# Performance work log

Hardware: AMD Instinct MI355X
Metric: run time of the kernel (lower is better)

Reference implementation:

```python
import jax, jax.numpy as jnp
import numpy as np

B, S, H, NH, FF, L = 2, 2048, 768, 12, 3072, 2
DH = H // NH
EPS = 1e-12
NEG = -10000.0


def setup_inputs() -> dict:
    key = jax.random.key(0)
    ks = jax.random.split(key, 10)
    w = lambda k, shp: jax.random.normal(k, shp, dtype=jnp.float32) * 0.02
    return {
        'hidden_states': jax.random.normal(ks[0], (B, S, H), dtype=jnp.float32),
        'attention_mask': jnp.ones((B, S), jnp.float32),
        'bias_matrix': jax.random.normal(ks[1], (S, S), dtype=jnp.float32) * 0.1,
        'bias_coef': jnp.ones((), jnp.float32),
        'Wq': w(ks[2], (L, H, H)), 'bq': jnp.zeros((L, H), jnp.float32),
        'Wk': w(ks[3], (L, H, H)), 'bk': jnp.zeros((L, H), jnp.float32),
        'Wv': w(ks[4], (L, H, H)), 'bv': jnp.zeros((L, H), jnp.float32),
        'Wo': w(ks[5], (L, H, H)), 'bo': jnp.zeros((L, H), jnp.float32),
        'ln1_g': jnp.ones((L, H), jnp.float32), 'ln1_b': jnp.zeros((L, H), jnp.float32),
        'Wi': w(ks[6], (L, H, FF)), 'bi': jnp.zeros((L, FF), jnp.float32),
        'Wo2': w(ks[7], (L, FF, H)), 'bo2': jnp.zeros((L, H), jnp.float32),
        'ln2_g': jnp.ones((L, H), jnp.float32), 'ln2_b': jnp.zeros((L, H), jnp.float32),
    }


def _layer_norm(x, g, b):
    mu = jnp.mean(x, axis=-1, keepdims=True)
    var = jnp.mean(jnp.square(x - mu), axis=-1, keepdims=True)
    return (x - mu) * jax.lax.rsqrt(var + EPS) * g + b


def reference(hidden_states, attention_mask, bias_matrix, bias_coef,
              Wq, bq, Wk, bk, Wv, bv, Wo, bo, ln1_g, ln1_b,
              Wi, bi, Wo2, bo2, ln2_g, ln2_b):
    # extended additive mask: [B,1,1,S]
    ext_mask = (1.0 - attention_mask)[:, None, None, :] * NEG
    bias = bias_matrix[None, None] * bias_coef  # [1,1,S,S]
    x = hidden_states
    scale = 1.0 / np.sqrt(DH)
    for i in range(L):
        q = (x @ Wq[i] + bq[i]).reshape(B, S, NH, DH).transpose(0, 2, 1, 3)
        k = (x @ Wk[i] + bk[i]).reshape(B, S, NH, DH).transpose(0, 2, 1, 3)
        v = (x @ Wv[i] + bv[i]).reshape(B, S, NH, DH).transpose(0, 2, 1, 3)
        scores = jnp.einsum('bhqd,bhkd->bhqk', q, k) * scale
        scores = scores + bias + ext_mask
        probs = jax.nn.softmax(scores, axis=-1)  # dropout = identity (eval)
        ctx = jnp.einsum('bhqk,bhkd->bhqd', probs, v)
        ctx = ctx.transpose(0, 2, 1, 3).reshape(B, S, H)
        attn_out = ctx @ Wo[i] + bo[i]
        x = _layer_norm(attn_out + x, ln1_g[i], ln1_b[i])
        inter = jax.nn.gelu(x @ Wi[i] + bi[i], approximate=False)
        ffn_out = inter @ Wo2[i] + bo2[i]
        x = _layer_norm(ffn_out + x, ln2_g[i], ln2_b[i])
    return x
```

## Files before the change

kernel.cpp:

```cpp
#include <hip/hip_runtime.h>
#include <hip/hip_bf16.h>
#include <math.h>

#define BB     2
#define SS     2048
#define HH     768
#define NHEAD  12
#define DHEAD  64
#define FFD    3072
#define NLAYER 2
#define MTOK   (BB*SS)
#define LOG2E  1.4426950408889634f
#define QSCALE 0.18033688011112042f

typedef __attribute__((ext_vector_type(8))) short bf16x8;
typedef __attribute__((ext_vector_type(4))) short bf16x4;
typedef __attribute__((ext_vector_type(4))) float f32x4;

__device__ __forceinline__ short f2bs(float f) {
    union { float f; unsigned u; } v; v.f = f;
    unsigned r = v.u + 0x7FFF + ((v.u >> 16) & 1);
    return (short)(r >> 16);
}
__device__ __forceinline__ float bs2f(short s) {
    union { unsigned u; float f; } v; v.u = ((unsigned)(unsigned short)s) << 16;
    return v.f;
}
__device__ __forceinline__ float fexp2(float x) {
    float r; asm("v_exp_f32 %0, %1" : "=v"(r) : "v"(x)); return r;
}
__device__ __forceinline__ void gl2lds16(const short* g, short* l) {
    __builtin_amdgcn_global_load_lds(
        (const __attribute__((address_space(1))) unsigned int*)g,
        (__attribute__((address_space(3))) unsigned int*)l, 16, 0, 0);
}

struct TJobs { const float* src[8]; short* dst[8]; };

__global__ __launch_bounds__(256)
void transpose_cvt_batch(TJobs jobs, int K, int N)
{
    const float* __restrict__ W  = jobs.src[blockIdx.z];
    short* __restrict__ Wt = jobs.dst[blockIdx.z];
    __shared__ short tile[32][33];
    const int k0 = blockIdx.x * 32, n0 = blockIdx.y * 32;
    const int tx = threadIdx.x & 31, ty = threadIdx.x >> 5;
#pragma unroll
    for (int i = 0; i < 4; i++)
        tile[ty + i*8][tx] = f2bs(W[(size_t)(k0 + ty + i*8) * N + n0 + tx]);
    __syncthreads();
#pragma unroll
    for (int i = 0; i < 4; i++)
        Wt[(size_t)(n0 + ty + i*8) * K + k0 + tx] = tile[tx][ty + i*8];
}

__global__ __launch_bounds__(256)
void cvt_bf16(const float* __restrict__ src, short* __restrict__ dst, int n)
{
    const int i = blockIdx.x * 256 + threadIdx.x;
    if (i < n) dst[i] = f2bs(src[i]);
}

__global__ __launch_bounds__(256)
void pack_bias(const float* __restrict__ bq, const float* __restrict__ bk,
               const float* __restrict__ bv, float* __restrict__ bqkv)
{
    const int t = blockIdx.x * 256 + threadIdx.x;
    if (t >= NLAYER * 2304) return;
    const int l = t / 2304, r = t % 2304;
    const float* src = (r < 768) ? bq : (r < 1536 ? bk : bv);
    bqkv[t] = src[l*768 + (r % 768)];
}

__global__ __launch_bounds__(256)
void bias_frag_prep(const float* __restrict__ biasM, const float* __restrict__ mask,
                    const float* __restrict__ coefp, short* __restrict__ bFrag)
{
    __shared__ float tile[64][129];
    const int tid = threadIdx.x;
    const int qb = blockIdx.x, q0 = qb*64, k0 = blockIdx.y*128;
#pragma unroll
    for (int p = 0; p < 8; p++) {
        const int row = p*8 + (tid >> 5);
        const int col = (tid & 31) * 4;
        float4 v = *(const float4*)&biasM[(size_t)(q0 + row)*SS + k0 + col];
        tile[row][col+0] = v.x; tile[row][col+1] = v.y;
        tile[row][col+2] = v.z; tile[row][col+3] = v.w;
    }
    __syncthreads();
    const float coef = coefp[0];
    const int lane = tid & 63, w = tid >> 6;
    const int l16 = lane & 15, g = lane >> 4;
    const int qrow = w*16 + l16;
#pragma unroll
    for (int b = 0; b < BB; b++) {
#pragma unroll
        for (int kt = 0; kt < 8; kt++) {
            bf16x4 o;
#pragma unroll
            for (int r = 0; r < 4; r++) {
                const int kk = kt*16 + g*4 + r;
                const float madd = (1.f - mask[b*SS + k0 + kk]) * (-10000.0f);
                o[r] = f2bs((tile[qrow][kk] * coef + madd) * LOG2E);
            }
            const size_t idx = ((((size_t)b*32 + qb)*4 + w)*128 + (k0>>4) + kt)*256 + lane*4;
            *(bf16x4*)&bFrag[idx] = o;
        }
    }
}

__global__ __launch_bounds__(256)
void gemm_mfma(const short* __restrict__ A, const short* __restrict__ Bt,
               const float* __restrict__ bias, short* __restrict__ C, int ldc,
               int M, int N, int K, int gelu, short* __restrict__ VtOut, int vsplit,
               float qscale, int qcols)
{
    __shared__ short sA[2][128*32];
    __shared__ short sB[2][128*32];
    const int tid  = threadIdx.x;
    const int w    = tid >> 6;
    const int lane = tid & 63;
    const int l16  = lane & 15, g = lane >> 4;
    const int wm   = w & 1, wn = w >> 1;
    const size_t m0 = (size_t)blockIdx.y * 128, n0 = (size_t)blockIdx.x * 128;

    const int srow = lane >> 2;
    const int kc   = lane & 3;

    f32x4 acc[4][4];
#pragma unroll
    for (int i = 0; i < 4; i++)
#pragma unroll
        for (int j = 0; j < 4; j++) acc[i][j] = (f32x4){0.f,0.f,0.f,0.f};

    const short* gA0 = A  + (m0 + w*32 +      srow) * (size_t)K + kc*8;
    const short* gA1 = A  + (m0 + w*32 + 16 + srow) * (size_t)K + kc*8;
    const short* gB0 = Bt + (n0 + w*32 +      srow) * (size_t)K + kc*8;
    const short* gB1 = Bt + (n0 + w*32 + 16 + srow) * (size_t)K + kc*8;
    const int oA0 = (w*32     )*32, oA1 = (w*32 + 16)*32;

    for (int k0 = 0; k0 < K; k0 += 64) {
        gl2lds16(gA0 + k0,      &sA[0][oA0]);
        gl2lds16(gA1 + k0,      &sA[0][oA1]);
        gl2lds16(gB0 + k0,      &sB[0][oA0]);
        gl2lds16(gB1 + k0,      &sB[0][oA1]);
        gl2lds16(gA0 + k0 + 32, &sA[1][oA0]);
        gl2lds16(gA1 + k0 + 32, &sA[1][oA1]);
        gl2lds16(gB0 + k0 + 32, &sB[1][oA0]);
        gl2lds16(gB1 + k0 + 32, &sB[1][oA1]);
        __syncthreads();

#pragma unroll
        for (int s = 0; s < 2; s++) {
            bf16x8 af[4], bfr[4];
#pragma unroll
            for (int mt = 0; mt < 4; mt++)
                af[mt] = *(const bf16x8*)&sA[s][(wm*64 + mt*16 + l16)*32 + g*8];
#pragma unroll
            for (int nt = 0; nt < 4; nt++)
                bfr[nt] = *(const bf16x8*)&sB[s][(wn*64 + nt*16 + l16)*32 + g*8];
#pragma unroll
            for (int mt = 0; mt < 4; mt++)
#pragma unroll
                for (int nt = 0; nt < 4; nt++)
                    acc[mt][nt] = __builtin_amdgcn_mfma_f32_16x16x32_bf16(
                                      af[mt], bfr[nt], acc[mt][nt], 0, 0, 0);
        }
        __syncthreads();
    }

#pragma unroll
    for (int mt = 0; mt < 4; mt++) {
        const size_t row0 = m0 + wm*64 + mt*16 + g*4;
#pragma unroll
        for (int nt = 0; nt < 4; nt++) {
            const size_t col = n0 + wn*64 + nt*16 + l16;
            if ((int)col >= vsplit) {
                short4 t;
                t.x = f2bs(acc[mt][nt][0] + bias[col]);
                t.y = f2bs(acc[mt][nt][1] + bias[col]);
                t.z = f2bs(acc[mt][nt][2] + bias[col]);
                t.w = f2bs(acc[mt][nt][3] + bias[col]);
                *(short4*)&VtOut[(size_t)(col - vsplit)*MTOK + row0] = t;
            } else {
#pragma unroll
                for (int r = 0; r < 4; r++) {
                    float v = acc[mt][nt][r] + bias[col];
                    if ((int)col < qcols) v *= qscale;
                    if (gelu) v = 0.5f * v * (1.f + erff(v * 0.70710678118f));
                    C[(row0 + r) * (size_t)ldc + col] = f2bs(v);
                }
            }
        }
    }
}

__global__ __launch_bounds__(256)
void gemm_n64_splitk(const short* __restrict__ A, const short* __restrict__ Bt,
                     float* __restrict__ P, int K)
{
    const int K2 = K >> 1;
    const int z  = blockIdx.z;
    __shared__ short sA[2][128*32];
    __shared__ short sB[2][64*32];
    const int tid  = threadIdx.x;
    const int w    = tid >> 6;
    const int lane = tid & 63;
    const int l16  = lane & 15, g = lane >> 4;
    const int wm   = w & 1, wn = w >> 1;
    const size_t m0 = (size_t)blockIdx.y * 128, n0 = (size_t)blockIdx.x * 64;

    const int srow = lane >> 2;
    const int kc   = lane & 3;

    f32x4 acc[4][2];
#pragma unroll
    for (int i = 0; i < 4; i++)
#pragma unroll
        for (int j = 0; j < 2; j++) acc[i][j] = (f32x4){0.f,0.f,0.f,0.f};

    const short* gA0 = A  + (m0 + w*32 +      srow) * (size_t)K + z*K2 + kc*8;
    const short* gA1 = A  + (m0 + w*32 + 16 + srow) * (size_t)K + z*K2 + kc*8;
    const short* gB0 = Bt + (n0 + w*16 +      srow) * (size_t)K + z*K2 + kc*8;
    const int oA0 = (w*32     )*32, oA1 = (w*32 + 16)*32, oB0 = (w*16)*32;

    for (int k0 = 0; k0 < K2; k0 += 64) {
        gl2lds16(gA0 + k0,      &sA[0][oA0]);
        gl2lds16(gA1 + k0,      &sA[0][oA1]);
        gl2lds16(gB0 + k0,      &sB[0][oB0]);
        gl2lds16(gA0 + k0 + 32, &sA[1][oA0]);
        gl2lds16(gA1 + k0 + 32, &sA[1][oA1]);
        gl2lds16(gB0 + k0 + 32, &sB[1][oB0]);
        __syncthreads();

#pragma unroll
        for (int s = 0; s < 2; s++) {
            bf16x8 af[4], bfr[2];
#pragma unroll
            for (int mt = 0; mt < 4; mt++)
                af[mt] = *(const bf16x8*)&sA[s][(wm*64 + mt*16 + l16)*32 + g*8];
#pragma unroll
            for (int nt = 0; nt < 2; nt++)
                bfr[nt] = *(const bf16x8*)&sB[s][(wn*32 + nt*16 + l16)*32 + g*8];
#pragma unroll
            for (int mt = 0; mt < 4; mt++)
#pragma unroll
                for (int nt = 0; nt < 2; nt++)
                    acc[mt][nt] = __builtin_amdgcn_mfma_f32_16x16x32_bf16(
                                      af[mt], bfr[nt], acc[mt][nt], 0, 0, 0);
        }
        __syncthreads();
    }

    float* Pz = P + (size_t)z * MTOK * HH;
#pragma unroll
    for (int mt = 0; mt < 4; mt++) {
        const size_t row0 = m0 + wm*64 + mt*16 + g*4;
#pragma unroll
        for (int nt = 0; nt < 2; nt++) {
            const size_t col = n0 + wn*32 + nt*16 + l16;
#pragma unroll
            for (int r = 0; r < 4; r++)
                Pz[(row0 + r) * (size_t)HH + col] = acc[mt][nt][r];
        }
    }
}

__global__ __launch_bounds__(256, 3)
void attn_fused(const short* __restrict__ QK, const short* __restrict__ Vt,
                const short* __restrict__ bFrag, short* __restrict__ CTX)
{
    __shared__ short sK[128*72];
    __shared__ short sV[64*136];

    const int qb  = blockIdx.x;
    const int q0  = qb * 64;
    const int h   = blockIdx.y;
    const int b   = blockIdx.z;
    const int tid = threadIdx.x;
    const int w   = tid >> 6;
    const int lane = tid & 63;
    const int l16 = lane & 15;
    const int g   = lane >> 4;

    const short* qrow = QK + ((size_t)(b*SS) + q0 + w*16 + l16) * 1536 + h*64;
    bf16x8 bQ0 = *(const bf16x8*)(qrow + g*8);
    bf16x8 bQ1 = *(const bf16x8*)(qrow + 32 + g*8);

    f32x4 O[4];
#pragma unroll
    for (int d = 0; d < 4; d++) O[d] = (f32x4){0.f,0.f,0.f,0.f};
    float m_q = -1e30f, l_q = 0.f;

    const int krow = tid >> 3, kch = tid & 7;
    const int vrow = tid >> 4, vch = tid & 15;
    const short* Kg = QK + ((size_t)(b*SS) + krow)*1536 + 768 + h*64 + kch*8;
    const short* Vg = Vt + ((size_t)(h*64 + vrow))*MTOK + b*SS + vch*8;
    const short* bF = bFrag + ((((size_t)b*32 + qb)*4 + w)*128)*256 + lane*4;

    bf16x8 kreg[4], vreg[4];
#pragma unroll
    for (int p = 0; p < 4; p++) {
        kreg[p] = *(const bf16x8*)(Kg + (size_t)(p*32)*1536);
        vreg[p] = *(const bf16x8*)(Vg + (size_t)(p*16)*MTOK);
    }

    for (int k0 = 0; k0 < SS; k0 += 128) {
        const short* bFt = bF + ((size_t)(k0 >> 4))*256;
        bf16x4 bb[8];
#pragma unroll
        for (int t = 0; t < 8; t++)
            bb[t] = *(const bf16x4*)(bFt + (size_t)t*256);

#pragma unroll
        for (int p = 0; p < 4; p++) {
            *(bf16x8*)&sK[(p*32 + krow)*72 + kch*8]   = kreg[p];
            *(bf16x8*)&sV[(p*16 + vrow)*136 + vch*8]  = vreg[p];
        }
        __syncthreads();

        if (k0 + 128 < SS) {
#pragma unroll
            for (int p = 0; p < 4; p++) {
                kreg[p] = *(const bf16x8*)(Kg + (size_t)(k0 + 128 + p*32)*1536);
                vreg[p] = *(const bf16x8*)(Vg + (size_t)(p*16)*MTOK + k0 + 128);
            }
        }

        float S[8][4];
#pragma unroll
        for (int t = 0; t < 8; t++) {
            bf16x8 aK0 = *(const bf16x8*)&sK[(t*16 + l16)*72 + g*8];
            bf16x8 aK1 = *(const bf16x8*)&sK[(t*16 + l16)*72 + 32 + g*8];
            f32x4 c = (f32x4){0.f,0.f,0.f,0.f};
            c = __builtin_amdgcn_mfma_f32_16x16x32_bf16(aK0, bQ0, c, 0, 0, 0);
            c = __builtin_amdgcn_mfma_f32_16x16x32_bf16(aK1, bQ1, c, 0, 0, 0);
#pragma unroll
            for (int r = 0; r < 4; r++)
                S[t][r] = c[r] + bs2f(bb[t][r]);
        }

        float tm[8];
#pragma unroll
        for (int t = 0; t < 8; t++)
            tm[t] = fmaxf(fmaxf(S[t][0], S[t][1]), fmaxf(S[t][2], S[t][3]));
        float mx = fmaxf(fmaxf(fmaxf(tm[0], tm[1]), fmaxf(tm[2], tm[3])),
                         fmaxf(fmaxf(tm[4], tm[5]), fmaxf(tm[6], tm[7])));
        mx = fmaxf(mx, __shfl_xor(mx, 16));
        mx = fmaxf(mx, __shfl_xor(mx, 32));
        const float mnew  = fmaxf(m_q, mx);
        const float alpha = fexp2(m_q - mnew);
        float ts[8];
#pragma unroll
        for (int t = 0; t < 8; t++) {
            float p0 = fexp2(S[t][0] - mnew);
            float p1 = fexp2(S[t][1] - mnew);
            float p2 = fexp2(S[t][2] - mnew);
            float p3 = fexp2(S[t][3] - mnew);
            S[t][0] = p0; S[t][1] = p1; S[t][2] = p2; S[t][3] = p3;
            ts[t] = (p0 + p1) + (p2 + p3);
        }
        float rs = ((ts[0] + ts[1]) + (ts[2] + ts[3]))
                 + ((ts[4] + ts[5]) + (ts[6] + ts[7]));
        rs += __shfl_xor(rs, 16);
        rs += __shfl_xor(rs, 32);
        l_q = l_q * alpha + rs;
        m_q = mnew;

#pragma unroll
        for (int r = 0; r < 4; r++) {
            const float ar = __shfl(alpha, g*4 + r);
#pragma unroll
            for (int d = 0; d < 4; d++) O[d][r] *= ar;
        }

#define PVU(u)                                                                 \
        {                                                                      \
            unsigned pa, pb, pc, pe;                                           \
            asm("v_cvt_pk_bf16_f32 %0, %1, %2" : "=v"(pa)                      \
                : "v"(S[2*(u)][0]),   "v"(S[2*(u)][1]));                       \
            asm("v_cvt_pk_bf16_f32 %0, %1, %2" : "=v"(pb)                      \
                : "v"(S[2*(u)][2]),   "v"(S[2*(u)][3]));                       \
            asm("v_cvt_pk_bf16_f32 %0, %1, %2" : "=v"(pc)                      \
                : "v"(S[2*(u)+1][0]), "v"(S[2*(u)+1][1]));                     \
            asm("v_cvt_pk_bf16_f32 %0, %1, %2" : "=v"(pe)                      \
                : "v"(S[2*(u)+1][2]), "v"(S[2*(u)+1][3]));                     \
            asm("v_permlane32_swap_b32 %0, %1" : "+v"(pa), "+v"(pc));          \
            asm("v_permlane16_swap_b32 %0, %1" : "+v"(pa), "+v"(pc));          \
            asm("v_permlane32_swap_b32 %0, %1" : "+v"(pb), "+v"(pe));          \
            asm("v_permlane16_swap_b32 %0, %1" : "+v"(pb), "+v"(pe));          \
            union { unsigned uw[4]; bf16x8 v; } P_;                            \
            P_.uw[0] = pa; P_.uw[1] = pb; P_.uw[2] = pc; P_.uw[3] = pe;        \
            _Pragma("unroll")                                                  \
            for (int d = 0; d < 4; d++) {                                      \
                bf16x8 vv = *(const bf16x8*)&sV[(d*16 + l16)*136 + (u)*32 + g*8]; \
                O[d] = __builtin_amdgcn_mfma_f32_16x16x32_bf16(                \
                           P_.v, vv, O[d], 0, 0, 0);                           \
            }                                                                  \
        }
        PVU(0)
        PVU(1)
        PVU(2)
        PVU(3)
#undef PVU

        __syncthreads();
    }

    float linv[4];
#pragma unroll
    for (int r = 0; r < 4; r++)
        linv[r] = 1.f / __shfl(l_q, g*4 + r);
#pragma unroll
    for (int d = 0; d < 4; d++)
#pragma unroll
        for (int r = 0; r < 4; r++)
            CTX[((size_t)(b*SS) + q0 + w*16 + g*4 + r)*HH + h*64 + d*16 + l16]
                = f2bs(O[d][r] * linv[r]);
}

__global__ __launch_bounds__(256)
void add_ln3(const float* __restrict__ P, const float* __restrict__ bvec,
             const short* __restrict__ R,
             const float* __restrict__ g, const float* __restrict__ beta,
             short* __restrict__ Out, float* __restrict__ OutF)
{
    const int lane = threadIdx.x & 63;
    const int row  = blockIdx.x * 4 + (threadIdx.x >> 6);
    const size_t base = (size_t)row * HH;
    const size_t sH = (size_t)MTOK * HH;

    float v[12];
    float s = 0.f;
#pragma unroll
    for (int p = 0; p < 3; p++) {
        const int c = p*256 + lane*4;
        float4 p0 = *(const float4*)&P[base + c];
        float4 p1 = *(const float4*)&P[sH + base + c];
        float4 bv4 = *(const float4*)&bvec[c];
        bf16x4 rv = *(const bf16x4*)&R[base + c];
        float x0 = p0.x + p1.x + bv4.x + bs2f(rv[0]);
        float x1 = p0.y + p1.y + bv4.y + bs2f(rv[1]);
        float x2 = p0.z + p1.z + bv4.z + bs2f(rv[2]);
        float x3 = p0.w + p1.w + bv4.w + bs2f(rv[3]);
        v[p*4+0] = x0; v[p*4+1] = x1; v[p*4+2] = x2; v[p*4+3] = x3;
        s += (x0 + x1) + (x2 + x3);
    }
    s += __shfl_xor(s, 1);  s += __shfl_xor(s, 2);  s += __shfl_xor(s, 4);
    s += __shfl_xor(s, 8);  s += __shfl_xor(s, 16); s += __shfl_xor(s, 32);
    const float mu = s * (1.f / HH);

    float s2 = 0.f;
#pragma unroll
    for (int j = 0; j < 12; j++) { float d = v[j] - mu; s2 += d * d; }
    s2 += __shfl_xor(s2, 1);  s2 += __shfl_xor(s2, 2);  s2 += __shfl_xor(s2, 4);
    s2 += __shfl_xor(s2, 8);  s2 += __shfl_xor(s2, 16); s2 += __shfl_xor(s2, 32);
    const float rstd = rsqrtf(s2 * (1.f / HH) + 1e-12f);

#pragma unroll
    for (int p = 0; p < 3; p++) {
        const int c = p*256 + lane*4;
        float4 gv = *(const float4*)&g[c];
        float4 bv = *(const float4*)&beta[c];
        float o0 = (v[p*4+0] - mu) * rstd * gv.x + bv.x;
        float o1 = (v[p*4+1] - mu) * rstd * gv.y + bv.y;
        float o2 = (v[p*4+2] - mu) * rstd * gv.z + bv.z;
        float o3 = (v[p*4+3] - mu) * rstd * gv.w + bv.w;
        bf16x4 ov; ov[0] = f2bs(o0); ov[1] = f2bs(o1); ov[2] = f2bs(o2); ov[3] = f2bs(o3);
        *(bf16x4*)&Out[base + c] = ov;
        if (OutF) {
            float4 of; of.x = o0; of.y = o1; of.z = o2; of.w = o3;
            *(float4*)&OutF[base + c] = of;
        }
    }
}

extern "C" void kernel_launch(void* const* d_in, const int* in_sizes, int n_in,
                              void* d_out, int out_size, void* d_ws, size_t ws_size,
                              hipStream_t stream)
{
    const float* hs    = (const float*)d_in[0];
    const float* mask  = (const float*)d_in[1];
    const float* biasM = (const float*)d_in[2];
    const float* coef  = (const float*)d_in[3];
    const float* Wq    = (const float*)d_in[4];
    const float* bq    = (const float*)d_in[5];
    const float* Wk    = (const float*)d_in[6];
    const float* bk    = (const float*)d_in[7];
    const float* Wv    = (const float*)d_in[8];
    const float* bv    = (const float*)d_in[9];
    const float* Wo    = (const float*)d_in[10];
    const float* bo    = (const float*)d_in[11];
    const float* ln1g  = (const float*)d_in[12];
    const float* ln1b  = (const float*)d_in[13];
    const float* Wi    = (const float*)d_in[14];
    const float* bi    = (const float*)d_in[15];
    const float* Wo2   = (const float*)d_in[16];
    const float* bo2   = (const float*)d_in[17];
    const float* ln2g  = (const float*)d_in[18];
    const float* ln2b  = (const float*)d_in[19];

    const size_t sH   = (size_t)MTOK * HH;
    const size_t sQK  = (size_t)MTOK * 1536;
    const size_t sVt  = (size_t)HH * MTOK;
    const size_t WPL  = 7077888;
    short* wt    = (short*)d_ws;
    float* bqkv  = (float*)(wt + 2*WPL);
    short* bFrag = (short*)(bqkv + 2*2304);
    short* X     = bFrag + (size_t)2*SS*SS;
    short* X2    = X  + sH;
    short* QK    = X2 + sH;
    short* Vt    = QK + sQK;
    short* CTX   = Vt + sVt;
    float* PK    = (float*)(CTX + sH);
    short* INTER = QK;

    const dim3 blk(256);

    TJobs jH, jI, jO;
    for (int l = 0; l < NLAYER; l++) {
        short* wl = wt + (size_t)l * WPL;
        jH.src[l*4+0] = Wq + (size_t)l*HH*HH;  jH.dst[l*4+0] = wl;
        jH.src[l*4+1] = Wk + (size_t)l*HH*HH;  jH.dst[l*4+1] = wl + 768*768;
        jH.src[l*4+2] = Wv + (size_t)l*HH*HH;  jH.dst[l*4+2] = wl + 1536*768;
        jH.src[l*4+3] = Wo + (size_t)l*HH*HH;  jH.dst[l*4+3] = wl + 1769472;
        jI.src[l] = Wi  + (size_t)l*HH*FFD;    jI.dst[l] = wl + 2359296;
        jO.src[l] = Wo2 + (size_t)l*FFD*HH;    jO.dst[l] = wl + 4718592;
    }
    transpose_cvt_batch<<<dim3(24,24,8), blk, 0, stream>>>(jH, HH, HH);
    transpose_cvt_batch<<<dim3(24,96,2), blk, 0, stream>>>(jI, HH, FFD);
    transpose_cvt_batch<<<dim3(96,24,2), blk, 0, stream>>>(jO, FFD, HH);
    bias_frag_prep<<<dim3(SS/64, SS/128), blk, 0, stream>>>(biasM, mask, coef, bFrag);
    pack_bias<<<dim3((NLAYER*2304 + 255)/256), blk, 0, stream>>>(bq, bk, bv, bqkv);
    cvt_bf16<<<dim3((int)((sH + 255)/256)), blk, 0, stream>>>(hs, X, (int)sH);

    const dim3 gQKV(2304/128, MTOK/128);
    const dim3 gSK (HH/64,    MTOK/128, 2);
    const dim3 gFF (FFD/128,  MTOK/128);
    const dim3 gA  (SS/64, NHEAD, BB);
    const dim3 gLN (MTOK/4);
    const int NOSPLIT = 1 << 30;

    for (int l = 0; l < NLAYER; l++) {
        short* wl = wt + (size_t)l * WPL;
        gemm_mfma<<<gQKV, blk, 0, stream>>>(X, wl, bqkv + l*2304, QK, 1536,
                                            MTOK, 2304, HH, 0, Vt, 1536,
                                            QSCALE, 768);
        attn_fused<<<gA, blk, 0, stream>>>(QK, Vt, bFrag, CTX);
        gemm_n64_splitk<<<gSK, blk, 0, stream>>>(CTX, wl + 1769472, PK, HH);
        add_ln3<<<gLN, blk, 0, stream>>>(PK, bo + l*HH, X, ln1g + l*HH, ln1b + l*HH,
                                         X2, nullptr);
        gemm_mfma<<<gFF, blk, 0, stream>>>(X2, wl + 2359296, bi + l*FFD, INTER, FFD,
                                           MTOK, FFD, HH, 1, nullptr, NOSPLIT,
                                           1.f, 0);
        gemm_n64_splitk<<<gSK, blk, 0, stream>>>(INTER, wl + 4718592, PK, FFD);
        add_ln3<<<gLN, blk, 0, stream>>>(PK, bo2 + l*HH, X2, ln2g + l*HH, ln2b + l*HH,
                                         X, (l == NLAYER-1) ? (float*)d_out : nullptr);
    }
}
```

Before: 555.3 us.

## Split attention over key halves with a separate merge kernel and lazy rescale

Splits each attention block's key range into two halves, doubling the grid so more blocks run at once. Each half writes unnormalized fp32 partial outputs plus the running max and sum to a workspace, and a new merge kernel combines them into the bf16 context. It also skips the output rescale when no row max grows in a wave, and raises the launch-bounds occupancy hint. The cost is extra fp32 partial-output traffic and one more kernel launch per layer.

```diff
diff --git a/kernel.cpp b/kernel.cpp
--- a/kernel.cpp
+++ b/kernel.cpp
@@ -266,22 +266,25 @@
     }
 }
 
-__global__ __launch_bounds__(256, 3)
+__global__ __launch_bounds__(256, 4)
 void attn_fused(const short* __restrict__ QK, const short* __restrict__ Vt,
-                const short* __restrict__ bFrag, short* __restrict__ CTX)
+                const short* __restrict__ bFrag, float* __restrict__ PO,
+                float2* __restrict__ ML)
 {
     __shared__ short sK[128*72];
     __shared__ short sV[64*136];
 
-    const int qb  = blockIdx.x;
-    const int q0  = qb * 64;
-    const int h   = blockIdx.y;
-    const int b   = blockIdx.z;
-    const int tid = threadIdx.x;
-    const int w   = tid >> 6;
+    const int qb   = blockIdx.x;
+    const int q0   = qb * 64;
+    const int h    = blockIdx.y;
+    const int b    = blockIdx.z >> 1;
+    const int half = blockIdx.z & 1;
+    const int koff = half * (SS/2);
+    const int tid  = threadIdx.x;
+    const int w    = tid >> 6;
     const int lane = tid & 63;
-    const int l16 = lane & 15;
-    const int g   = lane >> 4;
+    const int l16  = lane & 15;
+    const int g    = lane >> 4;
 
     const short* qrow = QK + ((size_t)(b*SS) + q0 + w*16 + l16) * 1536 + h*64;
     bf16x8 bQ0 = *(const bf16x8*)(qrow + g*8);
@@ -294,8 +297,8 @@
 
     const int krow = tid >> 3, kch = tid & 7;
     const int vrow = tid >> 4, vch = tid & 15;
-    const short* Kg = QK + ((size_t)(b*SS) + krow)*1536 + 768 + h*64 + kch*8;
-    const short* Vg = Vt + ((size_t)(h*64 + vrow))*MTOK + b*SS + vch*8;
+    const short* Kg = QK + ((size_t)(b*SS) + koff + krow)*1536 + 768 + h*64 + kch*8;
+    const short* Vg = Vt + ((size_t)(h*64 + vrow))*MTOK + b*SS + koff + vch*8;
     const short* bF = bFrag + ((((size_t)b*32 + qb)*4 + w)*128)*256 + lane*4;
 
     bf16x8 kreg[4], vreg[4];
@@ -305,8 +308,8 @@
         vreg[p] = *(const bf16x8*)(Vg + (size_t)(p*16)*MTOK);
     }
 
-    for (int k0 = 0; k0 < SS; k0 += 128) {
-        const short* bFt = bF + ((size_t)(k0 >> 4))*256;
+    for (int k0 = 0; k0 < SS/2; k0 += 128) {
+        const short* bFt = bF + ((size_t)((koff + k0) >> 4))*256;
         bf16x4 bb[8];
 #pragma unroll
         for (int t = 0; t < 8; t++)
@@ -319,7 +322,7 @@
         }
         __syncthreads();
 
-        if (k0 + 128 < SS) {
+        if (k0 + 128 < SS/2) {
 #pragma unroll
             for (int p = 0; p < 4; p++) {
                 kreg[p] = *(const bf16x8*)(Kg + (size_t)(k0 + 128 + p*32)*1536);
@@ -348,8 +351,10 @@
                          fmaxf(fmaxf(tm[4], tm[5]), fmaxf(tm[6], tm[7])));
         mx = fmaxf(mx, __shfl_xor(mx, 16));
         mx = fmaxf(mx, __shfl_xor(mx, 32));
-        const float mnew  = fmaxf(m_q, mx);
-        const float alpha = fexp2(m_q - mnew);
+
+        const bool grow = !__all(mx <= m_q);
+        const float mnew = grow ? fmaxf(m_q, mx) : m_q;
+
         float ts[8];
 #pragma unroll
         for (int t = 0; t < 8; t++) {
@@ -364,14 +369,19 @@
                  + ((ts[4] + ts[5]) + (ts[6] + ts[7]));
         rs += __shfl_xor(rs, 16);
         rs += __shfl_xor(rs, 32);
-        l_q = l_q * alpha + rs;
-        m_q = mnew;
-
-#pragma unroll
-        for (int r = 0; r < 4; r++) {
-            const float ar = __shfl(alpha, g*4 + r);
-#pragma unroll
-            for (int d = 0; d < 4; d++) O[d][r] *= ar;
+
+        if (grow) {
+            const float alpha = fexp2(m_q - mnew);
+            l_q = l_q * alpha + rs;
+            m_q = mnew;
+#pragma unroll
+            for (int r = 0; r < 4; r++) {
+                const float ar = __shfl(alpha, g*4 + r);
+#pragma unroll
+                for (int d = 0; d < 4; d++) O[d][r] *= ar;
+            }
+        } else {
+            l_q += rs;
         }
 
 #define PVU(u)                                                                 \
@@ -407,16 +417,47 @@
         __syncthreads();
     }
 
-    float linv[4];
-#pragma unroll
-    for (int r = 0; r < 4; r++)
-        linv[r] = 1.f / __shfl(l_q, g*4 + r);
+    float* PO_ = PO + (size_t)half * MTOK * HH;
 #pragma unroll
     for (int d = 0; d < 4; d++)
 #pragma unroll
         for (int r = 0; r < 4; r++)
-            CTX[((size_t)(b*SS) + q0 + w*16 + g*4 + r)*HH + h*64 + d*16 + l16]
-                = f2bs(O[d][r] * linv[r]);
+            PO_[((size_t)(b*SS) + q0 + w*16 + g*4 + r)*HH + h*64 + d*16 + l16]
+                = O[d][r];
+    if (g == 0) {
+        float2 ml; ml.x = m_q; ml.y = l_q;
+        ML[((size_t)half*MTOK + b*SS + q0 + w*16 + l16)*NHEAD + h] = ml;
+    }
+}
+
+__global__ __launch_bounds__(256)
+void add_merge(const float* __restrict__ PO, const float2* __restrict__ ML,
+               short* __restrict__ CTX)
+{
+    const int lane = threadIdx.x & 63;
+    const int row  = blockIdx.x * 4 + (threadIdx.x >> 6);
+    const size_t base = (size_t)row * HH;
+    const size_t sH = (size_t)MTOK * HH;
+
+#pragma unroll
+    for (int p = 0; p < 3; p++) {
+        const int c = p*256 + lane*4;
+        const int h = c >> 6;
+        float2 a = ML[(size_t)row*NHEAD + h];
+        float2 bm = ML[(size_t)MTOK*NHEAD + (size_t)row*NHEAD + h];
+        const float M  = fmaxf(a.x, bm.x);
+        const float w0 = fexp2(a.x - M);
+        const float w1 = fexp2(bm.x - M);
+        const float linv = 1.f / (a.y*w0 + bm.y*w1);
+        float4 p0 = *(const float4*)&PO[base + c];
+        float4 p1 = *(const float4*)&PO[sH + base + c];
+        bf16x4 ov;
+        ov[0] = f2bs((p0.x*w0 + p1.x*w1) * linv);
+        ov[1] = f2bs((p0.y*w0 + p1.y*w1) * linv);
+        ov[2] = f2bs((p0.z*w0 + p1.z*w1) * linv);
+        ov[3] = f2bs((p0.w*w0 + p1.w*w1) * linv);
+        *(bf16x4*)&CTX[base + c] = ov;
+    }
 }
 
 __global__ __launch_bounds__(256)
@@ -513,6 +554,7 @@
     short* Vt    = QK + sQK;
     short* CTX   = Vt + sVt;
     float* PK    = (float*)(CTX + sH);
+    float2* ML   = (float2*)(PK + 2*sH);
     short* INTER = QK;
 
     const dim3 blk(256);
@@ -537,7 +579,7 @@
     const dim3 gQKV(2304/128, MTOK/128);
     const dim3 gSK (HH/64,    MTOK/128, 2);
     const dim3 gFF (FFD/128,  MTOK/128);
-    const dim3 gA  (SS/64, NHEAD, BB);
+    const dim3 gA  (SS/64, NHEAD, BB*2);
     const dim3 gLN (MTOK/4);
     const int NOSPLIT = 1 << 30;
 
@@ -546,7 +588,8 @@
         gemm_mfma<<<gQKV, blk, 0, stream>>>(X, wl, bqkv + l*2304, QK, 1536,
                                             MTOK, 2304, HH, 0, Vt, 1536,
                                             QSCALE, 768);
-        attn_fused<<<gA, blk, 0, stream>>>(QK, Vt, bFrag, CTX);
+        attn_fused<<<gA, blk, 0, stream>>>(QK, Vt, bFrag, PK, ML);
+        add_merge<<<gLN, blk, 0, stream>>>(PK, ML, CTX);
         gemm_n64_splitk<<<gSK, blk, 0, stream>>>(CTX, wl + 1769472, PK, HH);
         add_ln3<<<gLN, blk, 0, stream>>>(PK, bo + l*HH, X, ln1g + l*HH, ln1b + l*HH,
                                          X2, nullptr);
```

Result: slower. 577.0 us (+3.9%).
